# Performance work log

Measured on AMD Instinct MI355X. Metric: run time of the kernel, lower is better.

## Reference

```python
import jax, jax.numpy as jnp
import numpy as np

EPS = 1e-5
H, HD = 8, 32  # n_heads, head_dim


def layer_norm(x, w, b):
    mu = jnp.mean(x, axis=-1, keepdims=True)
    var = jnp.mean(jnp.square(x - mu), axis=-1, keepdims=True)
    return (x - mu) * jax.lax.rsqrt(var + EPS) * w + b


def setup_inputs() -> dict:
    key = jax.random.key(0)
    ks = jax.random.split(key, 6)
    S, N, Dm, Dz = 256, 512, 64, 128
    return {
        "m": jax.random.normal(ks[0], (1, S, N, Dm), jnp.float32),
        "z": jax.random.normal(ks[1], (1, N, N, Dz), jnp.float32),
        "m_norm_w": jnp.ones((Dm,), jnp.float32),
        "m_norm_b": jnp.zeros((Dm,), jnp.float32),
        "z_norm_w": jnp.ones((Dz,), jnp.float32),
        "z_norm_b": jnp.zeros((Dz,), jnp.float32),
        "Wm": jax.random.normal(ks[2], (Dm, H * HD), jnp.float32) * 0.05,
        "Wg": jax.random.normal(ks[3], (Dm, H * HD), jnp.float32) * 0.05,
        "Wz": jax.random.normal(ks[4], (Dz, H), jnp.float32) * 0.05,
        "Wo": jax.random.normal(ks[5], (H * HD, Dm), jnp.float32) * 0.05,
    }


def reference(m, z, m_norm_w, m_norm_b, z_norm_w, z_norm_b, Wm, Wg, Wz, Wo):
    m0 = m[0]  # [S, N, Dm]
    z0 = z[0]  # [N, N, Dz]
    Dm = m0.shape[-1]
    mn = layer_norm(m0, m_norm_w, m_norm_b)
    zn = layer_norm(z0, z_norm_w, z_norm_b)
    # per-head softmax bias from pair rep: b[h,i,j]
    b = jnp.einsum('ijc,ch->hij', zn, Wz)
    w = jax.nn.softmax(b, axis=-1)  # [H, N, N]
    # values and gates: [S, N, H, HD]
    v = jnp.einsum('snc,chk->snhk', mn, Wm.reshape(Dm, H, HD))
    g = jax.nn.sigmoid(jnp.einsum('snc,chk->snhk', mn, Wg.reshape(Dm, H, HD)))
    # weighted averaging over tokens j
    o = jnp.einsum('hij,sjhk->sihk', w, v)  # [S, N, H, HD]
    out = jnp.einsum('sihk,hkc->sic', o * g, Wo.reshape(H, HD, Dm))
    return out[None]  # [1, S, N, Dm]
```

## Files before the change

### kernel.cpp

```cpp
#include <hip/hip_runtime.h>


#define S_DIM 256
#define N_DIM 512
#define DM 64
#define DZ 128
#define NH 8
#define HD 32
#define HK 256
#define NP 8192
#define BKP 32
#define JT_N 16

typedef unsigned int   u32;
typedef unsigned short u16;
typedef __bf16 bf16x8 __attribute__((ext_vector_type(8)));
typedef float  f32x4  __attribute__((ext_vector_type(4)));
typedef u32    u32x4  __attribute__((ext_vector_type(4)));

__device__ __forceinline__ u16 f2bf(float f) {
  u32 u = __builtin_bit_cast(u32, f);
  return (u16)((u + 0x7FFFu + ((u >> 16) & 1u)) >> 16);
}
__device__ __forceinline__ float bf2f(u16 h) {
  u32 u = ((u32)h) << 16;
  return __builtin_bit_cast(float, u);
}
__device__ __forceinline__ u32 pack2(float a, float b) {
  return (u32)f2bf(a) | ((u32)f2bf(b) << 16);
}
__device__ __forceinline__ bf16x8 ld8(const u16* p) {
  return __builtin_bit_cast(bf16x8, *(const u32x4*)p);
}
__device__ __forceinline__ f32x4 mfma16(bf16x8 a, bf16x8 b, f32x4 c) {
  return __builtin_amdgcn_mfma_f32_16x16x32_bf16(a, b, c, 0, 0, 0);
}
__device__ __forceinline__ void gload_lds16(const void* gsrc, void* ldst) {
  __builtin_amdgcn_global_load_lds(
      (const __attribute__((address_space(1))) void*)gsrc,
      (__attribute__((address_space(3))) void*)ldst, 16, 0, 0);
}
__device__ __forceinline__ float fast_sigmoid(float x) {
  float r;
  asm("v_rcp_f32 %0, %1" : "=v"(r) : "v"(1.f + __expf(-x)));
  return r;
}
__device__ __forceinline__ int swz(int lin) { return lin ^ (((lin >> 7) & 3) << 4); }

#define BARRIER() do { asm volatile("" ::: "memory"); \
                       __builtin_amdgcn_s_barrier();  \
                       asm volatile("" ::: "memory"); } while (0)

__global__ __launch_bounds__(256) void k0_prep(
    const float* __restrict__ Wm, const float* __restrict__ Wg,
    const float* __restrict__ Wo, const float* __restrict__ znw,
    const float* __restrict__ znb, const float* __restrict__ Wz,
    u16* __restrict__ wmg, u16* __restrict__ wof,
    u16* __restrict__ wzf, float* __restrict__ t1c) {
  const int idx = blockIdx.x * 256 + threadIdx.x;
  if (idx < 32768) {
    const int t = idx & 7, lane = (idx >> 3) & 63, ks = (idx >> 9) & 1, cb = idx >> 10;
    const int c = cb * 16 + (lane & 15);
    const int k = ks * 32 + ((lane >> 4) & 3) * 8 + t;
    const float v = (c < HK) ? Wm[k * HK + c] : Wg[k * HK + (c - HK)];
    wmg[idx] = f2bf(v);
  } else if (idx < 32768 + 16384) {
    const int j = idx - 32768;
    const int t = j & 7, lane = (j >> 3) & 63, ks = (j >> 9) & 7, cb = j >> 12;
    const int c = cb * 16 + (lane & 15);
    const int hk = ks * 32 + ((lane >> 4) & 3) * 8 + t;
    wof[j] = f2bf(Wo[hk * DM + c]);
  } else if (idx < 49152 + 4096) {
    const int q = idx - 49152;
    const int t = q & 7, lane = (q >> 3) & 63, p = (q >> 9) & 1, ks = q >> 10;
    const int h = lane & 15;
    const int k = ks * 32 + ((lane >> 4) & 3) * 8 + t;
    u16 val = 0;
    if (h < NH) {
      const float wp = znw[k] * Wz[k * NH + h];
      const u16 hi = f2bf(wp);
      val = (p == 0) ? hi : f2bf(wp - bf2f(hi));
    }
    wzf[q] = val;
  } else if (idx < 49152 + 4096 + 16) {
    const int q = idx - 49152 - 4096;
    const int h = q & 7;
    float s = 0.f;
    for (int c = 0; c < DZ; ++c)
      s += ((q < 8) ? znw[c] : znb[c]) * Wz[c * NH + h];
    t1c[q] = s;
  }
}

__global__ __launch_bounds__(512, 4) void k12_fused(
    const float* __restrict__ z, const u16* __restrict__ wzf,
    const float* __restrict__ t1c, u16* __restrict__ wout,
    const float* __restrict__ m, const float* __restrict__ mnw,
    const float* __restrict__ mnb, const u16* __restrict__ wmg,
    u16* __restrict__ mn, u16* __restrict__ vf) {
  __shared__ __attribute__((aligned(16))) float sB[NH][N_DIM + 4];
  const int tid = threadIdx.x, lane = tid & 63, wv = tid >> 6;

  if (blockIdx.x < 512) {
    const int i = blockIdx.x;
    const int h16 = lane & 15;
    const float t1 = t1c[h16 & 7], cst = t1c[8 + (h16 & 7)];

    for (int jj = 0; jj < 4; ++jj) {
      const float* zp = z + ((size_t)i * N_DIM + jj * 128 + wv * 16
                             + (lane & 15)) * DZ + ((lane >> 4) & 3) * 8;
      f32x4 acc = (f32x4){0.f, 0.f, 0.f, 0.f};
      float sum = 0.f, sq = 0.f;
      #pragma unroll
      for (int ks = 0; ks < 4; ++ks) {
        const float4 v0 = *(const float4*)(zp + ks * 32);
        const float4 v1 = *(const float4*)(zp + ks * 32 + 4);
        const float xs[8] = {v0.x, v0.y, v0.z, v0.w, v1.x, v1.y, v1.z, v1.w};
        bf16x8 zh, zl;
        #pragma unroll
        for (int t = 0; t < 8; ++t) {
          sum += xs[t]; sq += xs[t] * xs[t];
          const u16 hv = f2bf(xs[t]);
          ((u16*)&zh)[t] = hv;
          ((u16*)&zl)[t] = f2bf(xs[t] - bf2f(hv));
        }
        const bf16x8 wh = ld8(wzf + (ks * 2 + 0) * 512 + lane * 8);
        const bf16x8 wl = ld8(wzf + (ks * 2 + 1) * 512 + lane * 8);
        acc = mfma16(zh, wh, acc);
        acc = mfma16(zl, wh, acc);
        acc = mfma16(zh, wl, acc);
      }
      sum += __shfl_xor(sum, 16, 64); sum += __shfl_xor(sum, 32, 64);
      sq  += __shfl_xor(sq, 16, 64);  sq  += __shfl_xor(sq, 32, 64);
      const float mu = sum * (1.f / DZ);
      const float rs = rsqrtf(sq * (1.f / DZ) - mu * mu + 1e-5f);
      #pragma unroll
      for (int rg = 0; rg < 4; ++rg) {
        const int r = ((lane >> 4) & 3) * 4 + rg;
        const float mur = __shfl(mu, r, 64);
        const float rsr = __shfl(rs, r, 64);
        const float bv = rsr * (acc[rg] - mur * t1) + cst;
        if (h16 < NH) sB[h16][jj * 128 + wv * 16 + r] = bv;
      }
    }
    __syncthreads();

    {
      const int h = wv;
      const float* bp = &sB[h][lane * 8];
      const float4 v0 = *(const float4*)bp;
      const float4 v1 = *(const float4*)(bp + 4);
      float xs[8] = {v0.x, v0.y, v0.z, v0.w, v1.x, v1.y, v1.z, v1.w};
      float mx = xs[0];
      #pragma unroll
      for (int t = 1; t < 8; ++t) mx = fmaxf(mx, xs[t]);
      #pragma unroll
      for (int off = 32; off; off >>= 1) mx = fmaxf(mx, __shfl_xor(mx, off, 64));
      float sm = 0.f;
      #pragma unroll
      for (int t = 0; t < 8; ++t) { xs[t] = __expf(xs[t] - mx); sm += xs[t]; }
      #pragma unroll
      for (int off = 32; off; off >>= 1) sm += __shfl_xor(sm, off, 64);
      const float inv = 1.f / sm;
      u32x4 pk;
      pk[0] = pack2(xs[0] * inv, xs[1] * inv);
      pk[1] = pack2(xs[2] * inv, xs[3] * inv);
      pk[2] = pack2(xs[4] * inv, xs[5] * inv);
      pk[3] = pack2(xs[6] * inv, xs[7] * inv);
      *(u32x4*)(wout + (((size_t)(h * JT_N + (lane >> 2)) * N_DIM + i) << 5)
                + (lane & 3) * 8) = pk;
    }
  } else {
    float* swt = &sB[0][0];
    float* sbs = &sB[0][64];
    if (tid < DM) { swt[tid] = mnw[tid]; sbs[tid] = mnb[tid]; }
    __syncthreads();
    const int q = (lane >> 4) & 3;
    const int rbase = ((blockIdx.x - 512) * 8 + wv) * 16;
    const int r = rbase + (lane & 15);

    const float* mp = m + (size_t)r * DM + q * 8;
    const float4 va = *(const float4*)(mp);
    const float4 vb = *(const float4*)(mp + 4);
    const float4 vc = *(const float4*)(mp + 32);
    const float4 vd = *(const float4*)(mp + 36);
    const float x0[8] = {va.x, va.y, va.z, va.w, vb.x, vb.y, vb.z, vb.w};
    const float x1[8] = {vc.x, vc.y, vc.z, vc.w, vd.x, vd.y, vd.z, vd.w};
    float sum = 0.f, sq = 0.f;
    #pragma unroll
    for (int t = 0; t < 8; ++t) {
      sum += x0[t] + x1[t];
      sq  += x0[t] * x0[t] + x1[t] * x1[t];
    }
    sum += __shfl_xor(sum, 16, 64); sum += __shfl_xor(sum, 32, 64);
    sq  += __shfl_xor(sq, 16, 64);  sq  += __shfl_xor(sq, 32, 64);
    const float mu = sum * (1.f / DM);
    const float rs = rsqrtf(sq * (1.f / DM) - mu * mu + 1e-5f);

    bf16x8 a0, a1;
    #pragma unroll
    for (int t = 0; t < 8; ++t) {
      const int c0 = q * 8 + t, c1 = q * 8 + 32 + t;
      ((u16*)&a0)[t] = f2bf((x0[t] - mu) * rs * swt[c0] + sbs[c0]);
      ((u16*)&a1)[t] = f2bf((x1[t] - mu) * rs * swt[c1] + sbs[c1]);
    }
    *(u32x4*)(mn + (size_t)r * DM + q * 8)      = __builtin_bit_cast(u32x4, a0);
    *(u32x4*)(mn + (size_t)r * DM + q * 8 + 32) = __builtin_bit_cast(u32x4, a1);

    const u16* bp = wmg + lane * 8;
    const int r0 = rbase + ((lane >> 4) & 3) * 4;
    const int s0 = r0 >> 9;
    const int j0 = r0 & 511;

    f32x4 acc[16];
    #pragma unroll
    for (int cb = 0; cb < 16; ++cb) acc[cb] = (f32x4){0.f, 0.f, 0.f, 0.f};
    #pragma unroll
    for (int cb = 0; cb < 16; ++cb) {
      acc[cb] = mfma16(a0, ld8(bp + cb * 1024), acc[cb]);
      acc[cb] = mfma16(a1, ld8(bp + cb * 1024 + 512), acc[cb]);
    }
    #pragma unroll
    for (int cb = 0; cb < 16; ++cb) {
      const int c = cb * 16 + (lane & 15);
      const int h = c >> 5, k = c & 31;
      const int np = s0 * HD + k;
      const size_t idx = (((size_t)(h * JT_N + (j0 >> 5)) * NP + np) << 5) + (j0 & 31);
      ushort4 pk;
      pk.x = f2bf(acc[cb][0]); pk.y = f2bf(acc[cb][1]);
      pk.z = f2bf(acc[cb][2]); pk.w = f2bf(acc[cb][3]);
      *(ushort4*)(vf + idx) = pk;
    }
  }
}

__global__ __launch_bounds__(256, 4) void k3_fused(
    const u16* __restrict__ wf, const u16* __restrict__ vf,
    const u16* __restrict__ mn, const u16* __restrict__ wmg,
    const u16* __restrict__ wof, float* __restrict__ out) {
  __shared__ __attribute__((aligned(16))) u16 ring[4][4096];
  const int tid = threadIdx.x, lane = tid & 63, wv = tid >> 6;
  const int q = (lane >> 4) & 3;
  const int wr = wv >> 1, wc = wv & 1;
  const int bid = blockIdx.x;
  const int xcd = bid & 7, j = bid >> 3;
  const int xt = xcd * 16 + (j >> 3);
  const int yt = j & 7;
  const int i0 = yt * 64;
  const int n0 = xt * 64;
  const int s  = xt * 2 + wc;

  const int sbA = wv * 1024;
  const int soA = swz(sbA + lane * 16);
  const int soB = swz(sbA + lane * 16);

  int offA[2], offB[2];
  #pragma unroll
  for (int f = 0; f < 2; ++f)
    offA[f] = swz((wr * 32 + f * 16 + (lane & 15)) * 64 + q * 16);
  #pragma unroll
  for (int f = 0; f < 2; ++f)
    offB[f] = 4096 + swz((wc * 32 + f * 16 + (lane & 15)) * 64 + q * 16);

  bf16x8 mnf[2][2];
  #pragma unroll
  for (int fi = 0; fi < 2; ++fi) {
    const u16* mp_ = mn + (size_t)(s * N_DIM + i0 + wr * 32 + fi * 16
                                   + (lane & 15)) * DM + q * 8;
    mnf[fi][0] = ld8(mp_);
    mnf[fi][1] = ld8(mp_ + 32);
  }

  f32x4 acc[2][2];
  f32x4 oacc[4][2];
  #pragma unroll
  for (int a = 0; a < 2; ++a)
    #pragma unroll
    for (int b = 0; b < 2; ++b) acc[a][b] = (f32x4){0.f, 0.f, 0.f, 0.f};
  #pragma unroll
  for (int a = 0; a < 4; ++a)
    #pragma unroll
    for (int b = 0; b < 2; ++b) oacc[a][b] = (f32x4){0.f, 0.f, 0.f, 0.f};

  const char* gA = (const char*)(wf + (size_t)i0 * 32);
  const char* gB = (const char*)(vf + (size_t)n0 * 32);

#define STAGE_P(pA_, pB_, slot)                                            \
  do {                                                                     \
    char* dA_ = (char*)&ring[(slot)][0];                                   \
    gload_lds16((pA_) + soA, dA_ + sbA);                                   \
    gload_lds16((pB_) + soB, dA_ + 4096 + sbA);                            \
  } while (0)

#define COMPUTE(slot)                                                      \
  do {                                                                     \
    const char* cS_ = (const char*)&ring[(slot)][0];                       \
    bf16x8 af_[2], bf_[2];                                                 \
    _Pragma("unroll")                                                      \
    for (int f = 0; f < 2; ++f) af_[f] = ld8((const u16*)(cS_ + offA[f])); \
    _Pragma("unroll")                                                      \
    for (int f = 0; f < 2; ++f) bf_[f] = ld8((const u16*)(cS_ + offB[f])); \
    __builtin_amdgcn_s_setprio(1);                                         \
    _Pragma("unroll")                                                      \
    for (int fi = 0; fi < 2; ++fi)                                         \
      _Pragma("unroll")                                                    \
      for (int fn = 0; fn < 2; ++fn)                                       \
        acc[fi][fn] = mfma16(bf_[fn], af_[fi], acc[fi][fn]);               \
    __builtin_amdgcn_s_setprio(0);                                         \
  } while (0)

#define INTERLUDE(hh)                                                      \
  do {                                                                     \
    bf16x8 wg_[2][2];                                                      \
    _Pragma("unroll")                                                      \
    for (int k2 = 0; k2 < 2; ++k2)                                         \
      _Pragma("unroll")                                                    \
      for (int kk = 0; kk < 2; ++kk)                                       \
        wg_[k2][kk] = ld8(wmg + ((16 + (hh) * 2 + k2) * 2 + kk) * 512 + lane * 8); \
    u16* bb_ = &ring[2][0] + wv * 1024;                                    \
    _Pragma("unroll")                                                      \
    for (int fi = 0; fi < 2; ++fi) {                                       \
      const int row_ = fi * 16 + (lane & 15);                              \
      const int sw_ = (row_ & 3) << 3;                                     \
      _Pragma("unroll")                                                    \
      for (int fn = 0; fn < 2; ++fn) {                                     \
        f32x4 ga_ = (f32x4){0.f, 0.f, 0.f, 0.f};                           \
        ga_ = mfma16(wg_[fn][0], mnf[fi][0], ga_);                         \
        ga_ = mfma16(wg_[fn][1], mnf[fi][1], ga_);                         \
        ushort4 pk_;                                                       \
        pk_.x = f2bf(acc[fi][fn][0] * fast_sigmoid(ga_[0]));               \
        pk_.y = f2bf(acc[fi][fn][1] * fast_sigmoid(ga_[1]));               \
        pk_.z = f2bf(acc[fi][fn][2] * fast_sigmoid(ga_[2]));               \
        pk_.w = f2bf(acc[fi][fn][3] * fast_sigmoid(ga_[3]));               \
        *(ushort4*)(bb_ + row_ * 32 + ((fn * 16 + q * 4) ^ sw_)) = pk_;    \
        acc[fi][fn] = (f32x4){0.f, 0.f, 0.f, 0.f};                         \
      }                                                                    \
    }                                                                      \
    asm volatile("s_waitcnt lgkmcnt(0)" ::: "memory");                     \
    __builtin_amdgcn_sched_barrier(0);                                     \
    bf16x8 ogf_[2], wo_[4];                                                \
    _Pragma("unroll")                                                      \
    for (int fi = 0; fi < 2; ++fi) {                                       \
      const int row_ = fi * 16 + (lane & 15);                              \
      ogf_[fi] = ld8(bb_ + row_ * 32 + ((q * 8) ^ ((row_ & 3) << 3)));     \
    }                                                                      \
    _Pragma("unroll")                                                      \
    for (int cn = 0; cn < 4; ++cn)                                         \
      wo_[cn] = ld8(wof + ((cn * 8 + (hh)) * 64 + lane) * 8);              \
    _Pragma("unroll")                                                      \
    for (int cn = 0; cn < 4; ++cn)                                         \
      _Pragma("unroll")                                                    \
      for (int fi = 0; fi < 2; ++fi)                                       \
        oacc[cn][fi] = mfma16(wo_[cn], ogf_[fi], oacc[cn][fi]);            \
  } while (0)

  STAGE_P(gA, gB, 0);
  STAGE_P(gA + 32768, gB + 524288, 1);

  for (int ho = 0; ho < 7; ++ho) {
    const char* pAh = gA + (size_t)(ho * 16) * 32768;
    const char* pBh = gB + (size_t)(ho * 16) * 524288;
    #pragma unroll
    for (int u = 0; u < 16; ++u) {
      asm volatile("s_waitcnt vmcnt(2)" ::: "memory");
      BARRIER();
      STAGE_P(pAh + (size_t)(u + 2) * 32768, pBh + (size_t)(u + 2) * 524288,
              (u + 2) & 3);
      COMPUTE(u & 3);
    }
    INTERLUDE(ho);
  }
  {
    const char* pAh = gA + (size_t)112 * 32768;
    const char* pBh = gB + (size_t)112 * 524288;
    #pragma unroll
    for (int u = 0; u < 14; ++u) {
      asm volatile("s_waitcnt vmcnt(2)" ::: "memory");
      BARRIER();
      STAGE_P(pAh + (size_t)(u + 2) * 32768, pBh + (size_t)(u + 2) * 524288,
              (u + 2) & 3);
      COMPUTE(u & 3);
    }
    asm volatile("s_waitcnt vmcnt(2)" ::: "memory");
    BARRIER();
    COMPUTE(2);
    asm volatile("s_waitcnt vmcnt(0)" ::: "memory");
    BARRIER();
    COMPUTE(3);
    INTERLUDE(7);
  }
#undef STAGE_P
#undef COMPUTE
#undef INTERLUDE

  #pragma unroll
  for (int cn = 0; cn < 4; ++cn) {
    #pragma unroll
    for (int fi = 0; fi < 2; ++fi) {
      float* op = out + (size_t)(s * N_DIM + i0 + wr * 32 + fi * 16
                                 + (lane & 15)) * DM + cn * 16 + q * 4;
      *(f32x4*)op = oacc[cn][fi];
    }
  }
}

extern "C" void kernel_launch(void* const* d_in, const int* in_sizes, int n_in,
                              void* d_out, int out_size, void* d_ws, size_t ws_size,
                              hipStream_t stream) {
  const float* m   = (const float*)d_in[0];
  const float* z   = (const float*)d_in[1];
  const float* mnw = (const float*)d_in[2];
  const float* mnb = (const float*)d_in[3];
  const float* znw = (const float*)d_in[4];
  const float* znb = (const float*)d_in[5];
  const float* Wm  = (const float*)d_in[6];
  const float* Wg  = (const float*)d_in[7];
  const float* Wz  = (const float*)d_in[8];
  const float* Wo  = (const float*)d_in[9];
  float* out = (float*)d_out;
  char* ws = (char*)d_ws;

  u16*   wbuf = (u16*)(ws);
  u16*   vf   = (u16*)(ws + ((size_t)4   << 20));
  u16*   mn   = (u16*)(ws + ((size_t)132 << 20));
  u16*   wmg  = (u16*)(ws + ((size_t)148 << 20));
  u16*   wof  = (u16*)(ws + ((size_t)148 << 20) + 65536);
  u16*   wzf  = (u16*)(ws + ((size_t)148 << 20) + 98304);
  float* t1c  = (float*)(ws + ((size_t)148 << 20) + 106496);

  k0_prep<<<209, 256, 0, stream>>>(Wm, Wg, Wo, znw, znb, Wz, wmg, wof, wzf, t1c);
  k12_fused<<<1536, 512, 0, stream>>>(z, wzf, t1c, wbuf, m, mnw, mnb, wmg, mn, vf);
  k3_fused<<<1024, 256, 0, stream>>>(wbuf, vf, mn, wmg, wof, out);
}
```

Measured before the change: 121.9 us.

## Split fused softmax/value kernel and stage value tiles in LDS for coalesced stores

Result: slower. 128.5 us (+5.4%).

```diff
diff --git a/kernel.cpp b/kernel.cpp
--- a/kernel.cpp
+++ b/kernel.cpp
@@ -92,145 +92,152 @@
   }
 }
 
-__global__ __launch_bounds__(512, 4) void k12_fused(
+__global__ __launch_bounds__(512, 4) void k1_fused(
     const float* __restrict__ z, const u16* __restrict__ wzf,
-    const float* __restrict__ t1c, u16* __restrict__ wout,
+    const float* __restrict__ t1c, u16* __restrict__ wout) {
+  __shared__ __attribute__((aligned(16))) float sB[NH][N_DIM + 4];
+  const int tid = threadIdx.x, lane = tid & 63, wv = tid >> 6;
+  const int i = blockIdx.x;
+  const int h16 = lane & 15;
+  const float t1 = t1c[h16 & 7], cst = t1c[8 + (h16 & 7)];
+
+  for (int jj = 0; jj < 4; ++jj) {
+    const float* zp = z + ((size_t)i * N_DIM + jj * 128 + wv * 16
+                           + (lane & 15)) * DZ + ((lane >> 4) & 3) * 8;
+    f32x4 acc = (f32x4){0.f, 0.f, 0.f, 0.f};
+    float sum = 0.f, sq = 0.f;
+    #pragma unroll
+    for (int ks = 0; ks < 4; ++ks) {
+      const float4 v0 = *(const float4*)(zp + ks * 32);
+      const float4 v1 = *(const float4*)(zp + ks * 32 + 4);
+      const float xs[8] = {v0.x, v0.y, v0.z, v0.w, v1.x, v1.y, v1.z, v1.w};
+      bf16x8 zh, zl;
+      #pragma unroll
+      for (int t = 0; t < 8; ++t) {
+        sum += xs[t]; sq += xs[t] * xs[t];
+        const u16 hv = f2bf(xs[t]);
+        ((u16*)&zh)[t] = hv;
+        ((u16*)&zl)[t] = f2bf(xs[t] - bf2f(hv));
+      }
+      const bf16x8 wh = ld8(wzf + (ks * 2 + 0) * 512 + lane * 8);
+      const bf16x8 wl = ld8(wzf + (ks * 2 + 1) * 512 + lane * 8);
+      acc = mfma16(zh, wh, acc);
+      acc = mfma16(zl, wh, acc);
+      acc = mfma16(zh, wl, acc);
+    }
+    sum += __shfl_xor(sum, 16, 64); sum += __shfl_xor(sum, 32, 64);
+    sq  += __shfl_xor(sq, 16, 64);  sq  += __shfl_xor(sq, 32, 64);
+    const float mu = sum * (1.f / DZ);
+    const float rs = rsqrtf(sq * (1.f / DZ) - mu * mu + 1e-5f);
+    #pragma unroll
+    for (int rg = 0; rg < 4; ++rg) {
+      const int r = ((lane >> 4) & 3) * 4 + rg;
+      const float mur = __shfl(mu, r, 64);
+      const float rsr = __shfl(rs, r, 64);
+      const float bv = rsr * (acc[rg] - mur * t1) + cst;
+      if (h16 < NH) sB[h16][jj * 128 + wv * 16 + r] = bv;
+    }
+  }
+  __syncthreads();
+
+  {
+    const int h = wv;
+    const float* bp = &sB[h][lane * 8];
+    const float4 v0 = *(const float4*)bp;
+    const float4 v1 = *(const float4*)(bp + 4);
+    float xs[8] = {v0.x, v0.y, v0.z, v0.w, v1.x, v1.y, v1.z, v1.w};
+    float mx = xs[0];
+    #pragma unroll
+    for (int t = 1; t < 8; ++t) mx = fmaxf(mx, xs[t]);
+    #pragma unroll
+    for (int off = 32; off; off >>= 1) mx = fmaxf(mx, __shfl_xor(mx, off, 64));
+    float sm = 0.f;
+    #pragma unroll
+    for (int t = 0; t < 8; ++t) { xs[t] = __expf(xs[t] - mx); sm += xs[t]; }
+    #pragma unroll
+    for (int off = 32; off; off >>= 1) sm += __shfl_xor(sm, off, 64);
+    const float inv = 1.f / sm;
+    u32x4 pk;
+    pk[0] = pack2(xs[0] * inv, xs[1] * inv);
+    pk[1] = pack2(xs[2] * inv, xs[3] * inv);
+    pk[2] = pack2(xs[4] * inv, xs[5] * inv);
+    pk[3] = pack2(xs[6] * inv, xs[7] * inv);
+    *(u32x4*)(wout + (((size_t)(h * JT_N + (lane >> 2)) * N_DIM + i) << 5)
+              + (lane & 3) * 8) = pk;
+  }
+}
+
+__global__ __launch_bounds__(512, 2) void k2_fused(
     const float* __restrict__ m, const float* __restrict__ mnw,
     const float* __restrict__ mnb, const u16* __restrict__ wmg,
     u16* __restrict__ mn, u16* __restrict__ vf) {
-  __shared__ __attribute__((aligned(16))) float sB[NH][N_DIM + 4];
+  __shared__ u16 sv[32 * 32 * 34];
+  __shared__ float swt[DM], sbs[DM];
   const int tid = threadIdx.x, lane = tid & 63, wv = tid >> 6;
-
-  if (blockIdx.x < 512) {
-    const int i = blockIdx.x;
-    const int h16 = lane & 15;
-    const float t1 = t1c[h16 & 7], cst = t1c[8 + (h16 & 7)];
-
-    for (int jj = 0; jj < 4; ++jj) {
-      const float* zp = z + ((size_t)i * N_DIM + jj * 128 + wv * 16
-                             + (lane & 15)) * DZ + ((lane >> 4) & 3) * 8;
-      f32x4 acc = (f32x4){0.f, 0.f, 0.f, 0.f};
-      float sum = 0.f, sq = 0.f;
-      #pragma unroll
-      for (int ks = 0; ks < 4; ++ks) {
-        const float4 v0 = *(const float4*)(zp + ks * 32);
-        const float4 v1 = *(const float4*)(zp + ks * 32 + 4);
-        const float xs[8] = {v0.x, v0.y, v0.z, v0.w, v1.x, v1.y, v1.z, v1.w};
-        bf16x8 zh, zl;
-        #pragma unroll
-        for (int t = 0; t < 8; ++t) {
-          sum += xs[t]; sq += xs[t] * xs[t];
-          const u16 hv = f2bf(xs[t]);
-          ((u16*)&zh)[t] = hv;
-          ((u16*)&zl)[t] = f2bf(xs[t] - bf2f(hv));
-        }
-        const bf16x8 wh = ld8(wzf + (ks * 2 + 0) * 512 + lane * 8);
-        const bf16x8 wl = ld8(wzf + (ks * 2 + 1) * 512 + lane * 8);
-        acc = mfma16(zh, wh, acc);
-        acc = mfma16(zl, wh, acc);
-        acc = mfma16(zh, wl, acc);
-      }
-      sum += __shfl_xor(sum, 16, 64); sum += __shfl_xor(sum, 32, 64);
-      sq  += __shfl_xor(sq, 16, 64);  sq  += __shfl_xor(sq, 32, 64);
-      const float mu = sum * (1.f / DZ);
-      const float rs = rsqrtf(sq * (1.f / DZ) - mu * mu + 1e-5f);
-      #pragma unroll
-      for (int rg = 0; rg < 4; ++rg) {
-        const int r = ((lane >> 4) & 3) * 4 + rg;
-        const float mur = __shfl(mu, r, 64);
-        const float rsr = __shfl(rs, r, 64);
-        const float bv = rsr * (acc[rg] - mur * t1) + cst;
-        if (h16 < NH) sB[h16][jj * 128 + wv * 16 + r] = bv;
-      }
-    }
-    __syncthreads();
-
-    {
-      const int h = wv;
-      const float* bp = &sB[h][lane * 8];
-      const float4 v0 = *(const float4*)bp;
-      const float4 v1 = *(const float4*)(bp + 4);
-      float xs[8] = {v0.x, v0.y, v0.z, v0.w, v1.x, v1.y, v1.z, v1.w};
-      float mx = xs[0];
-      #pragma unroll
-      for (int t = 1; t < 8; ++t) mx = fmaxf(mx, xs[t]);
-      #pragma unroll
-      for (int off = 32; off; off >>= 1) mx = fmaxf(mx, __shfl_xor(mx, off, 64));
-      float sm = 0.f;
-      #pragma unroll
-      for (int t = 0; t < 8; ++t) { xs[t] = __expf(xs[t] - mx); sm += xs[t]; }
-      #pragma unroll
-      for (int off = 32; off; off >>= 1) sm += __shfl_xor(sm, off, 64);
-      const float inv = 1.f / sm;
-      u32x4 pk;
-      pk[0] = pack2(xs[0] * inv, xs[1] * inv);
-      pk[1] = pack2(xs[2] * inv, xs[3] * inv);
-      pk[2] = pack2(xs[4] * inv, xs[5] * inv);
-      pk[3] = pack2(xs[6] * inv, xs[7] * inv);
-      *(u32x4*)(wout + (((size_t)(h * JT_N + (lane >> 2)) * N_DIM + i) << 5)
-                + (lane & 3) * 8) = pk;
-    }
-  } else {
-    float* swt = &sB[0][0];
-    float* sbs = &sB[0][64];
-    if (tid < DM) { swt[tid] = mnw[tid]; sbs[tid] = mnb[tid]; }
-    __syncthreads();
-    const int q = (lane >> 4) & 3;
-    const int rbase = ((blockIdx.x - 512) * 8 + wv) * 16;
-    const int r = rbase + (lane & 15);
-
-    const float* mp = m + (size_t)r * DM + q * 8;
-    const float4 va = *(const float4*)(mp);
-    const float4 vb = *(const float4*)(mp + 4);
-    const float4 vc = *(const float4*)(mp + 32);
-    const float4 vd = *(const float4*)(mp + 36);
-    const float x0[8] = {va.x, va.y, va.z, va.w, vb.x, vb.y, vb.z, vb.w};
-    const float x1[8] = {vc.x, vc.y, vc.z, vc.w, vd.x, vd.y, vd.z, vd.w};
-    float sum = 0.f, sq = 0.f;
-    #pragma unroll
-    for (int t = 0; t < 8; ++t) {
-      sum += x0[t] + x1[t];
-      sq  += x0[t] * x0[t] + x1[t] * x1[t];
-    }
-    sum += __shfl_xor(sum, 16, 64); sum += __shfl_xor(sum, 32, 64);
-    sq  += __shfl_xor(sq, 16, 64);  sq  += __shfl_xor(sq, 32, 64);
-    const float mu = sum * (1.f / DM);
-    const float rs = rsqrtf(sq * (1.f / DM) - mu * mu + 1e-5f);
-
-    bf16x8 a0, a1;
-    #pragma unroll
-    for (int t = 0; t < 8; ++t) {
-      const int c0 = q * 8 + t, c1 = q * 8 + 32 + t;
-      ((u16*)&a0)[t] = f2bf((x0[t] - mu) * rs * swt[c0] + sbs[c0]);
-      ((u16*)&a1)[t] = f2bf((x1[t] - mu) * rs * swt[c1] + sbs[c1]);
-    }
-    *(u32x4*)(mn + (size_t)r * DM + q * 8)      = __builtin_bit_cast(u32x4, a0);
-    *(u32x4*)(mn + (size_t)r * DM + q * 8 + 32) = __builtin_bit_cast(u32x4, a1);
-
-    const u16* bp = wmg + lane * 8;
-    const int r0 = rbase + ((lane >> 4) & 3) * 4;
-    const int s0 = r0 >> 9;
-    const int j0 = r0 & 511;
-
-    f32x4 acc[16];
-    #pragma unroll
-    for (int cb = 0; cb < 16; ++cb) acc[cb] = (f32x4){0.f, 0.f, 0.f, 0.f};
-    #pragma unroll
-    for (int cb = 0; cb < 16; ++cb) {
-      acc[cb] = mfma16(a0, ld8(bp + cb * 1024), acc[cb]);
-      acc[cb] = mfma16(a1, ld8(bp + cb * 1024 + 512), acc[cb]);
-    }
-    #pragma unroll
-    for (int cb = 0; cb < 16; ++cb) {
-      const int c = cb * 16 + (lane & 15);
-      const int h = c >> 5, k = c & 31;
-      const int np = s0 * HD + k;
-      const size_t idx = (((size_t)(h * JT_N + (j0 >> 5)) * NP + np) << 5) + (j0 & 31);
-      ushort4 pk;
-      pk.x = f2bf(acc[cb][0]); pk.y = f2bf(acc[cb][1]);
-      pk.z = f2bf(acc[cb][2]); pk.w = f2bf(acc[cb][3]);
-      *(ushort4*)(vf + idx) = pk;
-    }
+  if (tid < DM) { swt[tid] = mnw[tid]; sbs[tid] = mnb[tid]; }
+  __syncthreads();
+  const int q = (lane >> 4) & 3;
+  const int bid = blockIdx.x;
+  const int rbase = (bid * 8 + wv) * 16;
+  const int r = rbase + (lane & 15);
+
+  const float* mp = m + (size_t)r * DM + q * 8;
+  const float4 va = *(const float4*)(mp);
+  const float4 vb = *(const float4*)(mp + 4);
+  const float4 vc = *(const float4*)(mp + 32);
+  const float4 vd = *(const float4*)(mp + 36);
+  const float x0[8] = {va.x, va.y, va.z, va.w, vb.x, vb.y, vb.z, vb.w};
+  const float x1[8] = {vc.x, vc.y, vc.z, vc.w, vd.x, vd.y, vd.z, vd.w};
+  float sum = 0.f, sq = 0.f;
+  #pragma unroll
+  for (int t = 0; t < 8; ++t) {
+    sum += x0[t] + x1[t];
+    sq  += x0[t] * x0[t] + x1[t] * x1[t];
+  }
+  sum += __shfl_xor(sum, 16, 64); sum += __shfl_xor(sum, 32, 64);
+  sq  += __shfl_xor(sq, 16, 64);  sq  += __shfl_xor(sq, 32, 64);
+  const float mu = sum * (1.f / DM);
+  const float rs = rsqrtf(sq * (1.f / DM) - mu * mu + 1e-5f);
+
+  bf16x8 a0, a1;
+  #pragma unroll
+  for (int t = 0; t < 8; ++t) {
+    const int c0 = q * 8 + t, c1 = q * 8 + 32 + t;
+    ((u16*)&a0)[t] = f2bf((x0[t] - mu) * rs * swt[c0] + sbs[c0]);
+    ((u16*)&a1)[t] = f2bf((x1[t] - mu) * rs * swt[c1] + sbs[c1]);
+  }
+  *(u32x4*)(mn + (size_t)r * DM + q * 8)      = __builtin_bit_cast(u32x4, a0);
+  *(u32x4*)(mn + (size_t)r * DM + q * 8 + 32) = __builtin_bit_cast(u32x4, a1);
+
+  const u16* bp = wmg + lane * 8;
+  const int jtl = wv >> 1;
+  const int jl0 = (wv & 1) * 16 + q * 4;
+  #pragma unroll
+  for (int cb = 0; cb < 16; ++cb) {
+    f32x4 acc = (f32x4){0.f, 0.f, 0.f, 0.f};
+    acc = mfma16(a0, ld8(bp + cb * 1024), acc);
+    acc = mfma16(a1, ld8(bp + cb * 1024 + 512), acc);
+    const int c = cb * 16 + (lane & 15);
+    const int h = c >> 5, k = c & 31;
+    ushort4 pk;
+    pk.x = f2bf(acc[0]); pk.y = f2bf(acc[1]);
+    pk.z = f2bf(acc[2]); pk.w = f2bf(acc[3]);
+    *(ushort4*)(&sv[((h * 4 + jtl) * 32 + k) * 34 + jl0]) = pk;
+  }
+  __syncthreads();
+
+  const int s0 = bid >> 2;
+  const int jtg0 = (bid & 3) * 4;
+  #pragma unroll
+  for (int cidx = 0; cidx < 8; ++cidx) {
+    const int ci = tid + cidx * 512;
+    const int p = ci >> 7, w = ci & 127;
+    const int h = p >> 2, jtl2 = p & 3;
+    const int k = w >> 2, j = (w & 3) * 8;
+    const u32x4 val = *(const u32x4*)(&sv[(p * 32 + k) * 34 + j]);
+    u16* dst = vf + ((size_t)(h * JT_N + jtg0 + jtl2) * NP << 5)
+               + s0 * 1024 + w * 8;
+    *(u32x4*)dst = val;
   }
 }
 
@@ -429,6 +436,7 @@
   float* t1c  = (float*)(ws + ((size_t)148 << 20) + 106496);
 
   k0_prep<<<209, 256, 0, stream>>>(Wm, Wg, Wo, znw, znb, Wz, wmg, wof, wzf, t1c);
-  k12_fused<<<1536, 512, 0, stream>>>(z, wzf, t1c, wbuf, m, mnw, mnb, wmg, mn, vf);
+  k1_fused<<<512, 512, 0, stream>>>(z, wzf, t1c, wbuf);
+  k2_fused<<<1024, 512, 0, stream>>>(m, mnw, mnb, wmg, mn, vf);
   k3_fused<<<1024, 256, 0, stream>>>(wbuf, vf, mn, wmg, wof, out);
 }
```
